# Performance work log

Hardware: AMD Instinct MI355X
Metric: run time of the kernel (lower is better)

Reference implementation:

```python
import jax, jax.numpy as jnp
import numpy as np

NHEAD, HD, ITERS = 8, 32, 6


def _layernorm(x, g, b, eps=1e-5):
    mu = jnp.mean(x, axis=-1, keepdims=True)
    var = jnp.mean((x - mu) ** 2, axis=-1, keepdims=True)
    return g * (x - mu) / jnp.sqrt(var + eps) + b


def _msa1(x, ax, WQ, bQ, WK, bK, WV, bV, WO, bO):
    # ring (sliding-window, size 3) attention + relay node as 4th key/value
    B, L, H = x.shape
    q = (x @ WQ + bQ).reshape(B, L, NHEAD, HD)
    k = (x @ WK + bK).reshape(B, L, NHEAD, HD)
    ak = (ax @ WK + bK).reshape(B, 1, NHEAD, 1, HD)   # relay key
    av = (ax @ WV + bV).reshape(B, 1, NHEAD, 1, HD)   # relay value
    padk = jnp.pad(k, ((0, 0), (1, 1), (0, 0), (0, 0)))
    wins = jnp.stack([padk[:, t:L + t] for t in range(3)], axis=3)  # [B,L,nh,3,hd]
    ak_b = jnp.broadcast_to(ak, (B, L, NHEAD, 1, HD))
    av_b = jnp.broadcast_to(av, (B, L, NHEAD, 1, HD))
    keys = jnp.concatenate([ak_b, wins], axis=3)   # [B,L,nh,4,hd]
    # NOTE: faithful to source bug: window VALUES come from k (pad_v = F.pad(k,...))
    vals = jnp.concatenate([av_b, wins], axis=3)
    scores = jnp.einsum('blnd,blnkd->blnk', q, keys) / np.sqrt(HD).astype(np.float32)
    alphas = jax.nn.softmax(scores, axis=-1)
    att = jnp.einsum('blnk,blnkd->blnd', alphas, vals).reshape(B, L, NHEAD * HD)
    return att @ WO + bO


def _msa2(x, y, WQ, bQ, WK, bK, WV, bV, WO, bO):
    # relay attends over [relay; nodes]; mask arg is ignored in the original
    B, L1, H = y.shape
    q = (x @ WQ + bQ).reshape(B, NHEAD, HD)
    k = (y @ WK + bK).reshape(B, L1, NHEAD, HD)
    v = (y @ WV + bV).reshape(B, L1, NHEAD, HD)
    scores = jnp.einsum('bnd,blnd->bnl', q, k) / np.sqrt(HD).astype(np.float32)
    alphas = jax.nn.softmax(scores, axis=-1)
    att = jnp.einsum('bnl,blnd->bnd', alphas, v).reshape(B, NHEAD * HD)
    return att @ WO + bO


def setup_inputs() -> dict:
    key = jax.random.key(0)
    ks = jax.random.split(key, 32)
    B, L, H, V, E, I = 32, 512, 256, 32000, 300, 6

    def rn(k, shape, s=0.05):
        return jax.random.normal(k, shape, jnp.float32) * s

    inp = {
        'data': jax.random.randint(ks[0], (B, L), 0, V),
        'emb': rn(ks[1], (V, E), 0.1),
        'emb_fc_W': rn(ks[2], (E, H)),
        'emb_fc_b': jnp.zeros((H,), jnp.float32),
        'pos_emb': rn(ks[3], (1000, H), 0.02),
        'ln_g': jnp.ones((I, H), jnp.float32),
        'ln_b': jnp.zeros((I, H), jnp.float32),
    }
    names = ['r_WQ', 'r_WK', 'r_WV', 'r_WO', 's_WQ', 's_WK', 's_WV', 's_WO']
    for j, n in enumerate(names):
        inp[n] = rn(ks[4 + j], (I, H, H))
        inp[n.replace('W', 'b')] = rn(ks[12 + j], (I, H), 0.01)
    return inp


def reference(data, emb, emb_fc_W, emb_fc_b, pos_emb, ln_g, ln_b,
              r_WQ, r_bQ, r_WK, r_bK, r_WV, r_bV, r_WO, r_bO,
              s_WQ, s_bQ, s_WK, s_bK, s_WV, s_bV, s_WO, s_bO):
    B, L = data.shape
    mask = (data == 1)
    e = emb[data]                                  # [B,L,nemb]
    P = pos_emb[:L][None]                          # [1,L,H]
    x0 = e @ emb_fc_W + emb_fc_b + P               # [B,L,H]
    nodes = x0
    relay = jnp.mean(x0, axis=1)                   # [B,H]
    for i in range(ITERS):
        ax = relay
        n_ln = _layernorm(nodes, ln_g[i], ln_b[i])
        nodes = nodes + jax.nn.leaky_relu(
            _msa1(n_ln, ax, r_WQ[i], r_bQ[i], r_WK[i], r_bK[i],
                  r_WV[i], r_bV[i], r_WO[i], r_bO[i]))
        y = jnp.concatenate([relay[:, None, :], nodes], axis=1)
        relay = jax.nn.leaky_relu(
            _msa2(relay, y, s_WQ[i], s_bQ[i], s_WK[i], s_bK[i],
                  s_WV[i], s_bV[i], s_WO[i], s_bO[i]))
        nodes = jnp.where(mask[:, :, None], 0.0, nodes)
    rep = 0.5 * jnp.max(nodes, axis=1) + 0.5 * relay
    return rep
```

## Files before the change

kernel.cpp:

```cpp
#include <hip/hip_runtime.h>
#include <stdint.h>

typedef __bf16 bf16x8 __attribute__((ext_vector_type(8)));
typedef unsigned short ushort8 __attribute__((ext_vector_type(8)));
typedef float floatx4 __attribute__((ext_vector_type(4)));

__device__ __forceinline__ unsigned short f2b(float f) {
    unsigned int u = __builtin_bit_cast(unsigned int, f);
    u += 0x7fffu + ((u >> 16) & 1u);
    return (unsigned short)(u >> 16);
}
__device__ __forceinline__ float b2f(unsigned short u) {
    union { unsigned int i; float f; } x; x.i = ((unsigned int)u) << 16; return x.f;
}
__device__ __forceinline__ void gl_lds16(const unsigned short* g, unsigned short* l) {
    __builtin_amdgcn_global_load_lds(
        (const __attribute__((address_space(1))) unsigned int*)g,
        (__attribute__((address_space(3))) unsigned int*)l, 16, 0, 0);
}

#define SCALE_QK 0.17677669529663687f

__global__ void transpose_many(const float* __restrict__ w0,
                               const float* __restrict__ w1,
                               const float* __restrict__ w2,
                               const float* __restrict__ w3,
                               const float* __restrict__ w4,
                               unsigned short* __restrict__ out) {
    int m = blockIdx.y;
    int fam = m / 6, it = m % 6;
    const float* src =
        (fam == 0 ? w0 : fam == 1 ? w1 : fam == 2 ? w2 : fam == 3 ? w3 : w4) + it * 65536;
    int e = blockIdx.x * 256 + threadIdx.x;
    int n = e >> 8, k = e & 255;
    out[(size_t)(it * 5 + fam) * 65536 + e] = f2b(src[k * 256 + n]);
}

__global__ void transpose_emb(const float* __restrict__ W,
                              unsigned short* __restrict__ out) {
    int e = blockIdx.x * 256 + threadIdx.x;
    int n = e / 320, k = e % 320;
    out[e] = (k < 300) ? f2b(W[k * 256 + n]) : (unsigned short)0;
}

__global__ void gather_emb(const int* __restrict__ data,
                           const float* __restrict__ emb,
                           unsigned short* __restrict__ apad) {
    int row = blockIdx.x;
    int tok = data[row];
    const float* er = emb + (size_t)tok * 300;
    for (int c = threadIdx.x; c < 320; c += 256)
        apad[(size_t)row * 320 + c] = (c < 300) ? f2b(er[c]) : (unsigned short)0;
}

template <int EPI, int KDIM>
__global__ __launch_bounds__(256) void gemm_k(const unsigned short* __restrict__ A,
                                              const unsigned short* __restrict__ Bt,
                                              const float* __restrict__ bias0,
                                              const float* __restrict__ bias1,
                                              float* __restrict__ outF,
                                              unsigned short* __restrict__ outB0,
                                              unsigned short* __restrict__ outB1,
                                              const float* __restrict__ pos,
                                              const int* __restrict__ dmask,
                                              int applyMask) {
    constexpr int G = KDIM / 8;
    __shared__ unsigned short Asm[64 * KDIM];
    __shared__ unsigned short Bsm[64 * KDIM];
    const int tid = threadIdx.x;
    const int wave = tid >> 6, lane = tid & 63;
    const int wm = (wave >> 1) * 32, wn = (wave & 1) * 32;
    const int quad = lane >> 4, l16 = lane & 15;
    const int rowBase = blockIdx.x * 64, colBase = blockIdx.y * 64;

    {
        const unsigned short* gbA = A + (size_t)(rowBase + wave * 16) * KDIM;
        const unsigned short* gbB = Bt + (size_t)(colBase + wave * 16) * KDIM;
        unsigned short* lbA = Asm + wave * 16 * KDIM;
        unsigned short* lbB = Bsm + wave * 16 * KDIM;
#pragma unroll
        for (int c = 0; c < G / 4; c++) {
            int gi = c * 64 + lane;
            int rl = gi / G, sl = gi - rl * G;
            int sg = sl ^ (rl & 7);
            gl_lds16(gbA + rl * KDIM + sg * 8, lbA + gi * 8);
            gl_lds16(gbB + rl * KDIM + sg * 8, lbB + gi * 8);
        }
    }
    __syncthreads();

    floatx4 acc[2][2] = {};
    const int mr0 = wm + l16, mr1 = wm + 16 + l16;
    const int nr0 = wn + l16, nr1 = wn + 16 + l16;
#pragma unroll
    for (int ks = 0; ks < KDIM / 32; ks++) {
        int g = ks * 4 + quad;
        bf16x8 af0 = __builtin_bit_cast(bf16x8, *(const ushort8*)&Asm[mr0 * KDIM + ((g ^ (mr0 & 7)) * 8)]);
        bf16x8 af1 = __builtin_bit_cast(bf16x8, *(const ushort8*)&Asm[mr1 * KDIM + ((g ^ (mr1 & 7)) * 8)]);
        bf16x8 bf0 = __builtin_bit_cast(bf16x8, *(const ushort8*)&Bsm[nr0 * KDIM + ((g ^ (nr0 & 7)) * 8)]);
        bf16x8 bf1 = __builtin_bit_cast(bf16x8, *(const ushort8*)&Bsm[nr1 * KDIM + ((g ^ (nr1 & 7)) * 8)]);
        acc[0][0] = __builtin_amdgcn_mfma_f32_16x16x32_bf16(af0, bf0, acc[0][0], 0, 0, 0);
        acc[0][1] = __builtin_amdgcn_mfma_f32_16x16x32_bf16(af0, bf1, acc[0][1], 0, 0, 0);
        acc[1][0] = __builtin_amdgcn_mfma_f32_16x16x32_bf16(af1, bf0, acc[1][0], 0, 0, 0);
        acc[1][1] = __builtin_amdgcn_mfma_f32_16x16x32_bf16(af1, bf1, acc[1][1], 0, 0, 0);
    }
    const int group = colBase >> 8;
    const float* bias = (EPI == 0 && group) ? bias1 : bias0;
    unsigned short* obf = (EPI == 0 && group) ? outB1 : outB0;
#pragma unroll
    for (int tm = 0; tm < 2; tm++) {
#pragma unroll
        for (int tn = 0; tn < 2; tn++) {
            int col = colBase + wn + tn * 16 + l16;
            int lc = col & 255;
            float bv = bias[lc];
#pragma unroll
            for (int r = 0; r < 4; r++) {
                int row = rowBase + wm + tm * 16 + quad * 4 + r;
                float c = acc[tm][tn][r] + bv;
                size_t o = (size_t)row * 256 + lc;
                if (EPI == 0) {
                    obf[o] = f2b(c);
                } else if (EPI == 1) {
                    float v = c > 0.f ? c : 0.01f * c;
                    float base = outF[o];
                    if (applyMask && dmask[row] == 1) base = 0.f;
                    float rr = base + v;
                    outF[o] = rr;
                    outB0[o] = f2b(rr);
                } else {
                    outF[o] = c + pos[(row & 511) * 256 + lc];
                }
            }
        }
    }
}

__global__ void mean_part(const float* __restrict__ nodes, float* __restrict__ part) {
    int b = blockIdx.x, c = blockIdx.y, h = threadIdx.x;
    const float* p = nodes + ((size_t)b * 512 + c * 32) * 256 + h;
    float s = 0.f;
    for (int l = 0; l < 32; l++) s += p[l * 256];
    part[(b * 16 + c) * 256 + h] = s;
}
__global__ void mean_comb(const float* __restrict__ part, float* __restrict__ relay) {
    int b = blockIdx.x, h = threadIdx.x;
    float s = 0.f;
    for (int c = 0; c < 16; c++) s += part[(b * 16 + c) * 256 + h];
    relay[b * 256 + h] = s * (1.f / 512.f);
}

__global__ __launch_bounds__(256) void ln_k(const float* __restrict__ nodes,
                                            const float* __restrict__ g,
                                            const float* __restrict__ bb,
                                            unsigned short* __restrict__ out,
                                            const int* __restrict__ dmask,
                                            int applyMask) {
    __shared__ float red[8];
    int row = blockIdx.x, t = threadIdx.x;
    int wv = t >> 6, ln_ = t & 63;
    float x = nodes[(size_t)row * 256 + t];
    if (applyMask && dmask[row] == 1) x = 0.f;
    float s = x;
#pragma unroll
    for (int o = 32; o; o >>= 1) s += __shfl_xor(s, o);
    if (ln_ == 0) red[wv] = s;
    __syncthreads();
    float mu = (red[0] + red[1] + red[2] + red[3]) * (1.f / 256.f);
    float d = x - mu;
    float v = d * d;
#pragma unroll
    for (int o = 32; o; o >>= 1) v += __shfl_xor(v, o);
    if (ln_ == 0) red[4 + wv] = v;
    __syncthreads();
    float var = (red[4] + red[5] + red[6] + red[7]) * (1.f / 256.f);
    float inv = rsqrtf(var + 1e-5f);
    out[(size_t)row * 256 + t] = f2b(g[t] * d * inv + bb[t]);
}

__global__ void relay5(const float* __restrict__ relay,
                       const float* __restrict__ rWK, const float* __restrict__ rbK,
                       const float* __restrict__ rWV, const float* __restrict__ rbV,
                       const float* __restrict__ sWQ, const float* __restrict__ sbQ,
                       const float* __restrict__ sWK, const float* __restrict__ sbK,
                       const float* __restrict__ sWV, const float* __restrict__ sbV,
                       float* __restrict__ AK, float* __restrict__ AV,
                       float* __restrict__ Q2, float* __restrict__ RK2, float* __restrict__ RV2) {
    __shared__ float r[256];
    int b = blockIdx.x, fam = blockIdx.y, t = threadIdx.x;
    r[t] = relay[b * 256 + t];
    __syncthreads();
    const float* W; const float* bi; float* o;
    switch (fam) {
        case 0: W = rWK; bi = rbK; o = AK; break;
        case 1: W = rWV; bi = rbV; o = AV; break;
        case 2: W = sWQ; bi = sbQ; o = Q2; break;
        case 3: W = sWK; bi = sbK; o = RK2; break;
        default: W = sWV; bi = sbV; o = RV2; break;
    }
    float s = 0.f;
    for (int e = 0; e < 256; e++) s += r[e] * W[e * 256 + t];
    o[b * 256 + t] = s + bi[t];
}

__global__ __launch_bounds__(256) void attn1_k(const unsigned short* __restrict__ q,
                                               const unsigned short* __restrict__ k,
                                               const float* __restrict__ ak,
                                               const float* __restrict__ av,
                                               unsigned short* __restrict__ att) {
    int tid = threadIdx.x;
    int row = blockIdx.x * 4 + (tid >> 6);
    int b = row >> 9, l = row & 511;
    int t = tid & 63;
    size_t o = (size_t)row * 256 + t * 4;
    ushort4 z4; z4.x = z4.y = z4.z = z4.w = 0;
    ushort4 q4 = *(const ushort4*)(q + o);
    ushort4 k04 = *(const ushort4*)(k + o);
    ushort4 km4 = (l > 0) ? *(const ushort4*)(k + o - 256) : z4;
    ushort4 kp4 = (l < 511) ? *(const ushort4*)(k + o + 256) : z4;
    float4 akv = *(const float4*)(ak + b * 256 + t * 4);
    float4 avv = *(const float4*)(av + b * 256 + t * 4);
    float qv0 = b2f(q4.x), qv1 = b2f(q4.y), qv2 = b2f(q4.z), qv3 = b2f(q4.w);
    float k00 = b2f(k04.x), k01 = b2f(k04.y), k02 = b2f(k04.z), k03 = b2f(k04.w);
    float km0 = b2f(km4.x), km1 = b2f(km4.y), km2 = b2f(km4.z), km3 = b2f(km4.w);
    float kp0 = b2f(kp4.x), kp1 = b2f(kp4.y), kp2 = b2f(kp4.z), kp3 = b2f(kp4.w);
    float s0 = qv0 * akv.x + qv1 * akv.y + qv2 * akv.z + qv3 * akv.w;
    float s1 = qv0 * km0 + qv1 * km1 + qv2 * km2 + qv3 * km3;
    float s2 = qv0 * k00 + qv1 * k01 + qv2 * k02 + qv3 * k03;
    float s3 = qv0 * kp0 + qv1 * kp1 + qv2 * kp2 + qv3 * kp3;
#pragma unroll
    for (int off = 4; off; off >>= 1) {
        s0 += __shfl_xor(s0, off);
        s1 += __shfl_xor(s1, off);
        s2 += __shfl_xor(s2, off);
        s3 += __shfl_xor(s3, off);
    }
    s0 *= SCALE_QK; s1 *= SCALE_QK; s2 *= SCALE_QK; s3 *= SCALE_QK;
    float m = fmaxf(fmaxf(s0, s1), fmaxf(s2, s3));
    float e0 = __expf(s0 - m), e1 = __expf(s1 - m), e2 = __expf(s2 - m), e3 = __expf(s3 - m);
    float iZ = 1.f / (e0 + e1 + e2 + e3);
    ushort4 r4;
    r4.x = f2b((e0 * avv.x + e1 * km0 + e2 * k00 + e3 * kp0) * iZ);
    r4.y = f2b((e0 * avv.y + e1 * km1 + e2 * k01 + e3 * kp1) * iZ);
    r4.z = f2b((e0 * avv.z + e1 * km2 + e2 * k02 + e3 * kp2) * iZ);
    r4.w = f2b((e0 * avv.w + e1 * km3 + e2 * k03 + e3 * kp3) * iZ);
    *(ushort4*)(att + o) = r4;
}

__global__ __launch_bounds__(256) void attn2_k(const float* __restrict__ q2,
                                               const unsigned short* __restrict__ k2,
                                               const unsigned short* __restrict__ v2,
                                               const float* __restrict__ rk2,
                                               const float* __restrict__ rv2,
                                               float* __restrict__ att2) {
    __shared__ float sc[513];
    __shared__ float qs[32];
    __shared__ float red[16];
    __shared__ float red2[256];
    int bn = blockIdx.x;
    int b = bn >> 3, n = bn & 7;
    int t = threadIdx.x;
    if (t < 32) qs[t] = q2[b * 256 + n * 32 + t];
    __syncthreads();
    float lmax = -1e30f;
    for (int li = t; li < 513; li += 256) {
        float d = 0.f;
        if (li == 0) {
            const float* kr = rk2 + b * 256 + n * 32;
#pragma unroll 8
            for (int j = 0; j < 32; j++) d += qs[j] * kr[j];
        } else {
            const unsigned short* kr = k2 + ((size_t)(b * 512 + li - 1) * 256 + n * 32);
#pragma unroll 8
            for (int j = 0; j < 32; j++) d += qs[j] * b2f(kr[j]);
        }
        d *= SCALE_QK;
        sc[li] = d;
        lmax = fmaxf(lmax, d);
    }
#pragma unroll
    for (int o = 32; o; o >>= 1) lmax = fmaxf(lmax, __shfl_xor(lmax, o));
    if ((t & 63) == 0) red[t >> 6] = lmax;
    __syncthreads();
    float m = fmaxf(fmaxf(red[0], red[1]), fmaxf(red[2], red[3]));
    float lsum = 0.f;
    for (int li = t; li < 513; li += 256) {
        float e = __expf(sc[li] - m);
        sc[li] = e;
        lsum += e;
    }
#pragma unroll
    for (int o = 32; o; o >>= 1) lsum += __shfl_xor(lsum, o);
    if ((t & 63) == 0) red[8 + (t >> 6)] = lsum;
    __syncthreads();
    float Z = red[8] + red[9] + red[10] + red[11];
    int d_ = t & 31, g_ = t >> 5;
    float acc = 0.f;
    for (int li = g_; li < 513; li += 8) {
        if (li == 0) {
            acc += sc[0] * rv2[b * 256 + n * 32 + d_];
        } else {
            acc += sc[li] * b2f(v2[(size_t)(b * 512 + li - 1) * 256 + n * 32 + d_]);
        }
    }
    red2[t] = acc;
    __syncthreads();
    if (t < 32) {
        float s = 0.f;
        for (int g = 0; g < 8; g++) s += red2[g * 32 + t];
        att2[b * 256 + n * 32 + t] = s / Z;
    }
}

__global__ void relay_out2(const float* __restrict__ att2,
                           const float* __restrict__ WO, const float* __restrict__ bO,
                           float* __restrict__ relay) {
    __shared__ float r[256];
    int b = blockIdx.x, t = threadIdx.x;
    r[t] = att2[b * 256 + t];
    __syncthreads();
    float s = 0.f;
    for (int e = 0; e < 256; e++) s += r[e] * WO[e * 256 + t];
    s += bO[t];
    relay[b * 256 + t] = s > 0.f ? s : 0.01f * s;
}

__global__ void rep_part(const float* __restrict__ nodes, const int* __restrict__ dmask,
                         float* __restrict__ part) {
    int b = blockIdx.x, c = blockIdx.y, h = threadIdx.x;
    const float* p = nodes + ((size_t)b * 512 + c * 32) * 256 + h;
    const int* dd = dmask + b * 512 + c * 32;
    float m = -1e30f;
    for (int l = 0; l < 32; l++) {
        float v = (dd[l] == 1) ? 0.f : p[l * 256];
        m = fmaxf(m, v);
    }
    part[(b * 16 + c) * 256 + h] = m;
}
__global__ void rep_comb(const float* __restrict__ part, const float* __restrict__ relay,
                         float* __restrict__ out) {
    int b = blockIdx.x, h = threadIdx.x;
    float m = -1e30f;
    for (int c = 0; c < 16; c++) m = fmaxf(m, part[(b * 16 + c) * 256 + h]);
    out[b * 256 + h] = 0.5f * m + 0.5f * relay[b * 256 + h];
}

extern "C" void kernel_launch(void* const* d_in, const int* in_sizes, int n_in,
                              void* d_out, int out_size, void* d_ws, size_t ws_size,
                              hipStream_t stream) {
    const int* data = (const int*)d_in[0];
    const float* emb = (const float*)d_in[1];
    const float* emb_fc_W = (const float*)d_in[2];
    const float* emb_fc_b = (const float*)d_in[3];
    const float* pos_emb = (const float*)d_in[4];
    const float* ln_g = (const float*)d_in[5];
    const float* ln_b = (const float*)d_in[6];
    const float* r_WQ = (const float*)d_in[7];
    const float* r_bQ = (const float*)d_in[8];
    const float* r_WK = (const float*)d_in[9];
    const float* r_bK = (const float*)d_in[10];
    const float* r_WV = (const float*)d_in[11];
    const float* r_bV = (const float*)d_in[12];
    const float* r_WO = (const float*)d_in[13];
    const float* r_bO = (const float*)d_in[14];
    const float* s_WQ = (const float*)d_in[15];
    const float* s_bQ = (const float*)d_in[16];
    const float* s_WK = (const float*)d_in[17];
    const float* s_bK = (const float*)d_in[18];
    const float* s_WV = (const float*)d_in[19];
    const float* s_bV = (const float*)d_in[20];
    const float* s_WO = (const float*)d_in[21];
    const float* s_bO = (const float*)d_in[22];

    char* w = (char*)d_ws;
    size_t off = 0;
    auto alloc = [&](size_t bytes) -> char* {
        char* p = w + off;
        off += (bytes + 255) & ~(size_t)255;
        return p;
    };
    float* RELAY = (float*)alloc(8192 * 4);
    float* AK = (float*)alloc(8192 * 4);
    float* AV = (float*)alloc(8192 * 4);
    float* Q2 = (float*)alloc(8192 * 4);
    float* RK2 = (float*)alloc(8192 * 4);
    float* RV2 = (float*)alloc(8192 * 4);
    float* ATT2 = (float*)alloc(8192 * 4);
    float* PART = (float*)alloc((size_t)32 * 16 * 256 * 4);
    unsigned short* WTE = (unsigned short*)alloc((size_t)256 * 320 * 2);
    unsigned short* WT = (unsigned short*)alloc((size_t)30 * 65536 * 2);
    float* NODES = (float*)alloc((size_t)16384 * 256 * 4);
    unsigned short* NLN = (unsigned short*)alloc((size_t)16384 * 256 * 2);
    unsigned short* Qb = (unsigned short*)alloc((size_t)16384 * 256 * 2);
    unsigned short* Kb16 = (unsigned short*)alloc((size_t)16384 * 256 * 2);
    unsigned short* NBF = (unsigned short*)alloc((size_t)16384 * 320 * 2);
    unsigned short* AEMB = NBF;
    unsigned short* ATT = NLN;
    unsigned short* K2b = Qb;
    unsigned short* V2b = Kb16;

    transpose_many<<<dim3(256, 30), 256, 0, stream>>>(r_WQ, r_WK, r_WO, s_WK, s_WV, WT);
    transpose_emb<<<320, 256, 0, stream>>>(emb_fc_W, WTE);
    gather_emb<<<16384, 256, 0, stream>>>(data, emb, AEMB);
    gemm_k<2, 320><<<dim3(256, 4), 256, 0, stream>>>(AEMB, WTE, emb_fc_b, nullptr,
                                                     NODES, nullptr, nullptr, pos_emb, nullptr, 0);
    mean_part<<<dim3(32, 16), 256, 0, stream>>>(NODES, PART);
    mean_comb<<<32, 256, 0, stream>>>(PART, RELAY);

    for (int i = 0; i < 6; i++) {
        const unsigned short* wQK = WT + (size_t)(i * 5 + 0) * 65536;
        const unsigned short* wO = WT + (size_t)(i * 5 + 2) * 65536;
        const unsigned short* wKV2 = WT + (size_t)(i * 5 + 3) * 65536;

        ln_k<<<16384, 256, 0, stream>>>(NODES, ln_g + i * 256, ln_b + i * 256, NLN, data, i > 0);
        gemm_k<0, 256><<<dim3(256, 8), 256, 0, stream>>>(NLN, wQK, r_bQ + i * 256, r_bK + i * 256,
                                                         nullptr, Qb, Kb16, nullptr, nullptr, 0);
        relay5<<<dim3(32, 5), 256, 0, stream>>>(RELAY,
                                                r_WK + (size_t)i * 65536, r_bK + i * 256,
                                                r_WV + (size_t)i * 65536, r_bV + i * 256,
                                                s_WQ + (size_t)i * 65536, s_bQ + i * 256,
                                                s_WK + (size_t)i * 65536, s_bK + i * 256,
                                                s_WV + (size_t)i * 65536, s_bV + i * 256,
                                                AK, AV, Q2, RK2, RV2);
        attn1_k<<<4096, 256, 0, stream>>>(Qb, Kb16, AK, AV, ATT);
        gemm_k<1, 256><<<dim3(256, 4), 256, 0, stream>>>(ATT, wO, r_bO + i * 256, nullptr,
                                                         NODES, NBF, nullptr, nullptr, data, i > 0);
        gemm_k<0, 256><<<dim3(256, 8), 256, 0, stream>>>(NBF, wKV2, s_bK + i * 256, s_bV + i * 256,
                                                         nullptr, K2b, V2b, nullptr, nullptr, 0);
        attn2_k<<<256, 256, 0, stream>>>(Q2, K2b, V2b, RK2, RV2, ATT2);
        relay_out2<<<32, 256, 0, stream>>>(ATT2, s_WO + (size_t)i * 65536, s_bO + i * 256, RELAY);
    }
    rep_part<<<dim3(32, 16), 256, 0, stream>>>(NODES, data, PART);
    rep_comb<<<32, 256, 0, stream>>>(PART, RELAY, (float*)d_out);
}
```

Baseline: 852.3 us.

## Tile weight transpose, stage GEMM bf16 output through LDS, widen small relay kernels

Replaces the per-element strided weight transpose with a 64x64 shared-memory tiled transpose so both reads and writes are coalesced. The EPI==0 GEMM epilogue now stages its bf16 results in LDS and writes 16-byte vectors instead of scattered 2-byte stores. The relay5 and relay_out2 matvecs split the K dimension across 1024 threads and reduce partial sums in shared memory. attn2_k goes from 256 to 512 threads. These changes aim to cut uncoalesced memory traffic and the latency of the serial small kernels, at the cost of extra barriers and LDS use.

Result: faster. 753.2 us (-11.6%).

```diff
diff --git a/kernel.cpp b/kernel.cpp
--- a/kernel.cpp
+++ b/kernel.cpp
@@ -21,19 +21,32 @@
 
 #define SCALE_QK 0.17677669529663687f
 
-__global__ void transpose_many(const float* __restrict__ w0,
-                               const float* __restrict__ w1,
-                               const float* __restrict__ w2,
-                               const float* __restrict__ w3,
-                               const float* __restrict__ w4,
-                               unsigned short* __restrict__ out) {
+__global__ __launch_bounds__(256) void transpose_many(const float* __restrict__ w0,
+                                                      const float* __restrict__ w1,
+                                                      const float* __restrict__ w2,
+                                                      const float* __restrict__ w3,
+                                                      const float* __restrict__ w4,
+                                                      unsigned short* __restrict__ out) {
+    __shared__ float tile[64][65];
     int m = blockIdx.y;
     int fam = m / 6, it = m % 6;
     const float* src =
         (fam == 0 ? w0 : fam == 1 ? w1 : fam == 2 ? w2 : fam == 3 ? w3 : w4) + it * 65536;
-    int e = blockIdx.x * 256 + threadIdx.x;
-    int n = e >> 8, k = e & 255;
-    out[(size_t)(it * 5 + fam) * 65536 + e] = f2b(src[k * 256 + n]);
+    unsigned short* dst = out + (size_t)(it * 5 + fam) * 65536;
+    int k0 = (blockIdx.x & 3) * 64, n0 = (blockIdx.x >> 2) * 64;
+    int tid = threadIdx.x;
+    int rg = tid >> 6, cl = tid & 63;
+#pragma unroll
+    for (int i = 0; i < 16; i++) {
+        int kl = rg * 16 + i;
+        tile[kl][cl] = src[(k0 + kl) * 256 + n0 + cl];
+    }
+    __syncthreads();
+#pragma unroll
+    for (int i = 0; i < 16; i++) {
+        int nl = rg * 16 + i;
+        dst[(n0 + nl) * 256 + k0 + cl] = f2b(tile[cl][nl]);
+    }
 }
 
 __global__ void transpose_emb(const float* __restrict__ W,
@@ -72,7 +85,6 @@
     const int wm = (wave >> 1) * 32, wn = (wave & 1) * 32;
     const int quad = lane >> 4, l16 = lane & 15;
     const int rowBase = blockIdx.x * 64, colBase = blockIdx.y * 64;
-
     {
         const unsigned short* gbA = A + (size_t)(rowBase + wave * 16) * KDIM;
         const unsigned short* gbB = Bt + (size_t)(colBase + wave * 16) * KDIM;
@@ -104,32 +116,56 @@
         acc[1][0] = __builtin_amdgcn_mfma_f32_16x16x32_bf16(af1, bf0, acc[1][0], 0, 0, 0);
         acc[1][1] = __builtin_amdgcn_mfma_f32_16x16x32_bf16(af1, bf1, acc[1][1], 0, 0, 0);
     }
-    const int group = colBase >> 8;
-    const float* bias = (EPI == 0 && group) ? bias1 : bias0;
-    unsigned short* obf = (EPI == 0 && group) ? outB1 : outB0;
-#pragma unroll
-    for (int tm = 0; tm < 2; tm++) {
-#pragma unroll
-        for (int tn = 0; tn < 2; tn++) {
-            int col = colBase + wn + tn * 16 + l16;
-            int lc = col & 255;
-            float bv = bias[lc];
-#pragma unroll
-            for (int r = 0; r < 4; r++) {
-                int row = rowBase + wm + tm * 16 + quad * 4 + r;
-                float c = acc[tm][tn][r] + bv;
-                size_t o = (size_t)row * 256 + lc;
-                if (EPI == 0) {
-                    obf[o] = f2b(c);
-                } else if (EPI == 1) {
-                    float v = c > 0.f ? c : 0.01f * c;
-                    float base = outF[o];
-                    if (applyMask && dmask[row] == 1) base = 0.f;
-                    float rr = base + v;
-                    outF[o] = rr;
-                    outB0[o] = f2b(rr);
-                } else {
-                    outF[o] = c + pos[(row & 511) * 256 + lc];
+    if (EPI == 0) {
+        const int group = colBase >> 8;
+        const float* bias = group ? bias1 : bias0;
+        unsigned short* obf = group ? outB1 : outB0;
+        unsigned short* tile = Asm;
+        __syncthreads();
+#pragma unroll
+        for (int tm = 0; tm < 2; tm++) {
+#pragma unroll
+            for (int tn = 0; tn < 2; tn++) {
+                int lcl = wn + tn * 16 + l16;
+                float bv = bias[(colBase & 255) + lcl];
+#pragma unroll
+                for (int r = 0; r < 4; r++) {
+                    int rl = wm + tm * 16 + quad * 4 + r;
+                    tile[rl * 72 + lcl] = f2b(acc[tm][tn][r] + bv);
+                }
+            }
+        }
+        __syncthreads();
+#pragma unroll
+        for (int j = 0; j < 2; j++) {
+            int c = j * 256 + tid;
+            int rl = c >> 3, c8 = c & 7;
+            ushort8 v = *(const ushort8*)&tile[rl * 72 + c8 * 8];
+            *(ushort8*)(obf + (size_t)(rowBase + rl) * 256 + (colBase & 255) + c8 * 8) = v;
+        }
+    } else {
+#pragma unroll
+        for (int tm = 0; tm < 2; tm++) {
+#pragma unroll
+            for (int tn = 0; tn < 2; tn++) {
+                int col = colBase + wn + tn * 16 + l16;
+                int lc = col & 255;
+                float bv = bias0[lc];
+#pragma unroll
+                for (int r = 0; r < 4; r++) {
+                    int row = rowBase + wm + tm * 16 + quad * 4 + r;
+                    float c = acc[tm][tn][r] + bv;
+                    size_t o = (size_t)row * 256 + lc;
+                    if (EPI == 1) {
+                        float v = c > 0.f ? c : 0.01f * c;
+                        float base = outF[o];
+                        if (applyMask && dmask[row] == 1) base = 0.f;
+                        float rr = base + v;
+                        outF[o] = rr;
+                        outB0[o] = f2b(rr);
+                    } else {
+                        outF[o] = c + pos[(row & 511) * 256 + lc];
+                    }
                 }
             }
         }
@@ -178,7 +214,7 @@
     out[(size_t)row * 256 + t] = f2b(g[t] * d * inv + bb[t]);
 }
 
-__global__ void relay5(const float* __restrict__ relay,
+__global__ __launch_bounds__(1024) void relay5(const float* __restrict__ relay,
                        const float* __restrict__ rWK, const float* __restrict__ rbK,
                        const float* __restrict__ rWV, const float* __restrict__ rbV,
                        const float* __restrict__ sWQ, const float* __restrict__ sbQ,
@@ -187,8 +223,9 @@
                        float* __restrict__ AK, float* __restrict__ AV,
                        float* __restrict__ Q2, float* __restrict__ RK2, float* __restrict__ RV2) {
     __shared__ float r[256];
+    __shared__ float part[1024];
     int b = blockIdx.x, fam = blockIdx.y, t = threadIdx.x;
-    r[t] = relay[b * 256 + t];
+    if (t < 256) r[t] = relay[b * 256 + t];
     __syncthreads();
     const float* W; const float* bi; float* o;
     switch (fam) {
@@ -198,9 +235,13 @@
         case 3: W = sWK; bi = sbK; o = RK2; break;
         default: W = sWV; bi = sbV; o = RV2; break;
     }
+    int col = t & 255, kc = t >> 8;
     float s = 0.f;
-    for (int e = 0; e < 256; e++) s += r[e] * W[e * 256 + t];
-    o[b * 256 + t] = s + bi[t];
+    for (int e = kc * 64; e < kc * 64 + 64; e++) s += r[e] * W[e * 256 + col];
+    part[t] = s;
+    __syncthreads();
+    if (kc == 0)
+        o[b * 256 + col] = part[col] + part[256 + col] + part[512 + col] + part[768 + col] + bi[col];
 }
 
 __global__ __launch_bounds__(256) void attn1_k(const unsigned short* __restrict__ q,
@@ -247,7 +288,7 @@
     *(ushort4*)(att + o) = r4;
 }
 
-__global__ __launch_bounds__(256) void attn2_k(const float* __restrict__ q2,
+__global__ __launch_bounds__(512) void attn2_k(const float* __restrict__ q2,
                                                const unsigned short* __restrict__ k2,
                                                const unsigned short* __restrict__ v2,
                                                const float* __restrict__ rk2,
@@ -256,14 +297,14 @@
     __shared__ float sc[513];
     __shared__ float qs[32];
     __shared__ float red[16];
-    __shared__ float red2[256];
+    __shared__ float red2[512];
     int bn = blockIdx.x;
     int b = bn >> 3, n = bn & 7;
     int t = threadIdx.x;
     if (t < 32) qs[t] = q2[b * 256 + n * 32 + t];
     __syncthreads();
     float lmax = -1e30f;
-    for (int li = t; li < 513; li += 256) {
+    for (int li = t; li < 513; li += 512) {
         float d = 0.f;
         if (li == 0) {
             const float* kr = rk2 + b * 256 + n * 32;
@@ -282,9 +323,11 @@
     for (int o = 32; o; o >>= 1) lmax = fmaxf(lmax, __shfl_xor(lmax, o));
     if ((t & 63) == 0) red[t >> 6] = lmax;
     __syncthreads();
-    float m = fmaxf(fmaxf(red[0], red[1]), fmaxf(red[2], red[3]));
+    float m = red[0];
+#pragma unroll
+    for (int i = 1; i < 8; i++) m = fmaxf(m, red[i]);
     float lsum = 0.f;
-    for (int li = t; li < 513; li += 256) {
+    for (int li = t; li < 513; li += 512) {
         float e = __expf(sc[li] - m);
         sc[li] = e;
         lsum += e;
@@ -293,10 +336,12 @@
     for (int o = 32; o; o >>= 1) lsum += __shfl_xor(lsum, o);
     if ((t & 63) == 0) red[8 + (t >> 6)] = lsum;
     __syncthreads();
-    float Z = red[8] + red[9] + red[10] + red[11];
+    float Z = red[8];
+#pragma unroll
+    for (int i = 9; i < 16; i++) Z += red[i];
     int d_ = t & 31, g_ = t >> 5;
     float acc = 0.f;
-    for (int li = g_; li < 513; li += 8) {
+    for (int li = g_; li < 513; li += 16) {
         if (li == 0) {
             acc += sc[0] * rv2[b * 256 + n * 32 + d_];
         } else {
@@ -307,22 +352,29 @@
     __syncthreads();
     if (t < 32) {
         float s = 0.f;
-        for (int g = 0; g < 8; g++) s += red2[g * 32 + t];
+#pragma unroll
+        for (int g = 0; g < 16; g++) s += red2[g * 32 + t];
         att2[b * 256 + n * 32 + t] = s / Z;
     }
 }
 
-__global__ void relay_out2(const float* __restrict__ att2,
+__global__ __launch_bounds__(1024) void relay_out2(const float* __restrict__ att2,
                            const float* __restrict__ WO, const float* __restrict__ bO,
                            float* __restrict__ relay) {
     __shared__ float r[256];
+    __shared__ float part[1024];
     int b = blockIdx.x, t = threadIdx.x;
-    r[t] = att2[b * 256 + t];
-    __syncthreads();
+    if (t < 256) r[t] = att2[b * 256 + t];
+    __syncthreads();
+    int col = t & 255, kc = t >> 8;
     float s = 0.f;
-    for (int e = 0; e < 256; e++) s += r[e] * WO[e * 256 + t];
-    s += bO[t];
-    relay[b * 256 + t] = s > 0.f ? s : 0.01f * s;
+    for (int e = kc * 64; e < kc * 64 + 64; e++) s += r[e] * WO[e * 256 + col];
+    part[t] = s;
+    __syncthreads();
+    if (kc == 0) {
+        float tot = part[col] + part[256 + col] + part[512 + col] + part[768 + col] + bO[col];
+        relay[b * 256 + col] = tot > 0.f ? tot : 0.01f * tot;
+    }
 }
 
 __global__ void rep_part(const float* __restrict__ nodes, const int* __restrict__ dmask,
@@ -399,7 +451,7 @@
     unsigned short* K2b = Qb;
     unsigned short* V2b = Kb16;
 
-    transpose_many<<<dim3(256, 30), 256, 0, stream>>>(r_WQ, r_WK, r_WO, s_WK, s_WV, WT);
+    transpose_many<<<dim3(16, 30), 256, 0, stream>>>(r_WQ, r_WK, r_WO, s_WK, s_WV, WT);
     transpose_emb<<<320, 256, 0, stream>>>(emb_fc_W, WTE);
     gather_emb<<<16384, 256, 0, stream>>>(data, emb, AEMB);
     gemm_k<2, 320><<<dim3(256, 4), 256, 0, stream>>>(AEMB, WTE, emb_fc_b, nullptr,
@@ -415,7 +467,7 @@
         ln_k<<<16384, 256, 0, stream>>>(NODES, ln_g + i * 256, ln_b + i * 256, NLN, data, i > 0);
         gemm_k<0, 256><<<dim3(256, 8), 256, 0, stream>>>(NLN, wQK, r_bQ + i * 256, r_bK + i * 256,
                                                          nullptr, Qb, Kb16, nullptr, nullptr, 0);
-        relay5<<<dim3(32, 5), 256, 0, stream>>>(RELAY,
+        relay5<<<dim3(32, 5), 1024, 0, stream>>>(RELAY,
                                                 r_WK + (size_t)i * 65536, r_bK + i * 256,
                                                 r_WV + (size_t)i * 65536, r_bV + i * 256,
                                                 s_WQ + (size_t)i * 65536, s_bQ + i * 256,
@@ -427,8 +479,8 @@
                                                          NODES, NBF, nullptr, nullptr, data, i > 0);
         gemm_k<0, 256><<<dim3(256, 8), 256, 0, stream>>>(NBF, wKV2, s_bK + i * 256, s_bV + i * 256,
                                                          nullptr, K2b, V2b, nullptr, nullptr, 0);
-        attn2_k<<<256, 256, 0, stream>>>(Q2, K2b, V2b, RK2, RV2, ATT2);
-        relay_out2<<<32, 256, 0, stream>>>(ATT2, s_WO + (size_t)i * 65536, s_bO + i * 256, RELAY);
+        attn2_k<<<256, 512, 0, stream>>>(Q2, K2b, V2b, RK2, RV2, ATT2);
+        relay_out2<<<32, 1024, 0, stream>>>(ATT2, s_WO + (size_t)i * 65536, s_bO + i * 256, RELAY);
     }
     rep_part<<<dim3(32, 16), 256, 0, stream>>>(NODES, data, PART);
     rep_comb<<<32, 256, 0, stream>>>(PART, RELAY, (float*)d_out);
```
